# Kernel tuning notes

Hardware: AMD Instinct MI355X
Metric: run time of the kernel (lower is better)

## Reference

```python
import jax, jax.numpy as jnp
import numpy as np

B, L, D = 1, 512, 1280


def setup_inputs() -> dict:
    key = jax.random.key(0)
    k1, k2, k3 = jax.random.split(key, 3)
    prev_result = jax.random.normal(k1, (B, L, D), dtype=jnp.float32)
    # nn.Linear(2*D, 2): store weight as [2D, 2] so forward is x @ W + b
    W = jax.random.normal(k2, (2 * D, 2), dtype=jnp.float32) * (1.0 / np.sqrt(2 * D))
    b = jax.random.normal(k3, (2,), dtype=jnp.float32) * 0.01
    return {"prev_result": prev_result, "W": W, "b": b}


def reference(prev_result, W, b):
    # Dropout is identity at inference. The torch code builds
    # pairwise = cat(x_i * x_j, x_i - x_j) of shape [B,L,L,2D] then applies
    # Linear(2D, 2). We fuse: split W into the prod half Wp and diff half Wd.
    Wp, Wd = W[:D], W[D:]                                   # each [D, 2]
    # (x_i * x_j) @ Wp  -- bilinear contraction, no [B,L,L,2D] intermediate
    prod_term = jnp.einsum('bid,bjd,dk->bijk', prev_result, prev_result, Wp)
    # (x_i - x_j) @ Wd = (x @ Wd)_i - (x @ Wd)_j
    d_proj = prev_result @ Wd                                # [B, L, 2]
    diff_term = d_proj[:, :, None, :] - d_proj[:, None, :, :]
    prediction = prod_term + diff_term + b                   # [B, L, L, 2]
    prediction = (prediction + prediction.transpose(0, 2, 1, 3)) / 2
    return prediction[:, 1:-1, 1:-1]                         # [B, L-2, L-2, 2]
```

## Files before the change

kernel.cpp:

```cpp
#include <hip/hip_runtime.h>
#include <math.h>

#define D_DIM 1280
#define ODIM  510
#define KSTEPS 40

typedef short bf16x8 __attribute__((ext_vector_type(8)));
typedef float f32x4  __attribute__((ext_vector_type(4)));

__device__ __forceinline__ unsigned pkbf(float a, float b) {
  unsigned ua = __float_as_uint(a), ub = __float_as_uint(b);
  return ((ua + 0x8000u) >> 16) | ((ub + 0x8000u) & 0xffff0000u);
}

__global__ __launch_bounds__(256, 1) void pcmd_prep(
    const float* __restrict__ X,
    const float* __restrict__ W,
    unsigned short* __restrict__ Xbf,
    unsigned short* __restrict__ A0,
    unsigned short* __restrict__ A1)
{
  int T = (int)blockIdx.x * 256 + (int)threadIdx.x;
  int r = T / 160;
  int c = T - r * 160;
  const int K = c >> 2, quad = c & 3, m = r & 15, R = r >> 4;
  const size_t g = ((size_t)(R * KSTEPS + K) * 64 + quad * 16 + m) * 8;

  uint4 vx = {0,0,0,0}, v0 = {0,0,0,0}, v1 = {0,0,0,0};
  if (r <= 510) {
    const float* px = X + (size_t)(r + 1) * D_DIM + c * 8;
    float4 x0 = *(const float4*)px;
    float4 x1 = *(const float4*)(px + 4);
    const float* pw = W + (size_t)c * 16;
    float4 w0 = *(const float4*)(pw +  0);
    float4 w1 = *(const float4*)(pw +  4);
    float4 w2 = *(const float4*)(pw +  8);
    float4 w3 = *(const float4*)(pw + 12);
    vx.x = pkbf(x0.x, x0.y);            vx.y = pkbf(x0.z, x0.w);
    vx.z = pkbf(x1.x, x1.y);            vx.w = pkbf(x1.z, x1.w);
    v0.x = pkbf(x0.x*w0.x, x0.y*w0.z);  v0.y = pkbf(x0.z*w1.x, x0.w*w1.z);
    v0.z = pkbf(x1.x*w2.x, x1.y*w2.z);  v0.w = pkbf(x1.z*w3.x, x1.w*w3.z);
    v1.x = pkbf(x0.x*w0.y, x0.y*w0.w);  v1.y = pkbf(x0.z*w1.y, x0.w*w1.w);
    v1.z = pkbf(x1.x*w2.y, x1.y*w2.w);  v1.w = pkbf(x1.z*w3.y, x1.w*w3.w);
  }
  *(uint4*)(Xbf + g) = vx;
  *(uint4*)(A0  + g) = v0;
  *(uint4*)(A1  + g) = v1;
}

__global__ __launch_bounds__(256, 2) void pcmd_gemm(
    const unsigned short* __restrict__ Xbf,
    const unsigned short* __restrict__ A0,
    const unsigned short* __restrict__ A1,
    const float* __restrict__ b,
    float* __restrict__ out)
{
  __shared__ float sR[4][2][16][17];

  const int t = (int)blockIdx.x;
  int bi = (int)((65.0 - sqrt(4225.0 - 8.0 * (double)t)) * 0.5);
  {
    int s0 = bi * 32 - (bi * (bi - 1)) / 2;
    if (t < s0) { --bi; }
    int s1 = (bi + 1) * 32 - ((bi + 1) * bi) / 2;
    if (t >= s1) { ++bi; }
  }
  const int start = bi * 32 - (bi * (bi - 1)) / 2;
  const int bj = bi + (t - start);

  const int tid  = threadIdx.x;
  const int lane = tid & 63;
  const int wv   = tid >> 6;

  const unsigned short* pa0 = A0  + ((size_t)(bi * KSTEPS + wv * 10) * 64 + lane) * 8;
  const unsigned short* pa1 = A1  + ((size_t)(bi * KSTEPS + wv * 10) * 64 + lane) * 8;
  const unsigned short* pb  = Xbf + ((size_t)(bj * KSTEPS + wv * 10) * 64 + lane) * 8;

  bf16x8 ra0[4], ra1[4], rb[4];
  #pragma unroll
  for (int s = 0; s < 4; ++s) {
    ra0[s] = *(const bf16x8*)(pa0 + s * 512);
    ra1[s] = *(const bf16x8*)(pa1 + s * 512);
    rb[s]  = *(const bf16x8*)(pb  + s * 512);
  }

  f32x4 acc0 = {0.f, 0.f, 0.f, 0.f};
  f32x4 acc1 = {0.f, 0.f, 0.f, 0.f};

  #pragma unroll
  for (int s = 0; s < 10; ++s) {
    const int cur = s & 3;
    bf16x8 a0 = ra0[cur], a1 = ra1[cur], bb = rb[cur];
    if (s + 4 < 10) {
      ra0[cur] = *(const bf16x8*)(pa0 + (s + 4) * 512);
      ra1[cur] = *(const bf16x8*)(pa1 + (s + 4) * 512);
      rb[cur]  = *(const bf16x8*)(pb  + (s + 4) * 512);
    }
    acc0 = __builtin_amdgcn_mfma_f32_16x16x32_bf16(a0, bb, acc0, 0, 0, 0);
    acc1 = __builtin_amdgcn_mfma_f32_16x16x32_bf16(a1, bb, acc1, 0, 0, 0);
  }

  const int m = lane & 15, quad = lane >> 4;
  #pragma unroll
  for (int r = 0; r < 4; ++r) {
    sR[wv][0][quad * 4 + r][m] = acc0[r];
    sR[wv][1][quad * 4 + r][m] = acc1[r];
  }
  __syncthreads();

  const float b0 = b[0], b1 = b[1];
  const int il = tid >> 4, jl = tid & 15;

  {
    const int oi = bi * 16 + il, oj = bj * 16 + jl;
    if (oi < ODIM && oj < ODIM) {
      float2 v;
      v.x = sR[0][0][il][jl] + sR[1][0][il][jl] + sR[2][0][il][jl] + sR[3][0][il][jl] + b0;
      v.y = sR[0][1][il][jl] + sR[1][1][il][jl] + sR[2][1][il][jl] + sR[3][1][il][jl] + b1;
      *(float2*)(out + ((size_t)oi * ODIM + oj) * 2) = v;
    }
  }
  if (bi != bj) {
    const int oi = bj * 16 + il, oj = bi * 16 + jl;
    if (oi < ODIM && oj < ODIM) {
      float2 v;
      v.x = sR[0][0][jl][il] + sR[1][0][jl][il] + sR[2][0][jl][il] + sR[3][0][jl][il] + b0;
      v.y = sR[0][1][jl][il] + sR[1][1][jl][il] + sR[2][1][jl][il] + sR[3][1][jl][il] + b1;
      *(float2*)(out + ((size_t)oi * ODIM + oj) * 2) = v;
    }
  }
}

extern "C" void kernel_launch(void* const* d_in, const int* in_sizes, int n_in,
                              void* d_out, int out_size, void* d_ws, size_t ws_size,
                              hipStream_t stream) {
  const float* X = (const float*)d_in[0];
  const float* W = (const float*)d_in[1];
  const float* b = (const float*)d_in[2];
  float* out = (float*)d_out;
  (void)in_sizes; (void)n_in; (void)out_size; (void)ws_size;

  const size_t PLANE = (size_t)512 * D_DIM;
  unsigned short* Xbf = (unsigned short*)d_ws;
  unsigned short* A0  = Xbf + PLANE;
  unsigned short* A1  = A0 + PLANE;

  hipLaunchKernelGGL(pcmd_prep, dim3(320), dim3(256), 0, stream, X, W, Xbf, A0, A1);
  hipLaunchKernelGGL(pcmd_gemm, dim3(528), dim3(256), 0, stream, Xbf, A0, A1, b, out);
}
```

Baseline: 70.50 us.

## Fuse bf16 prep into GEMM kernel, converting X tiles on the fly via LDS

Drops the separate prep kernel that wrote bf16 X and weight-scaled A0/A1 planes to workspace. Each GEMM block now loads fp32 X rows for its i and j tiles directly, scales by W staged in shared memory, packs to bf16 into a swizzled LDS buffer, and feeds the MFMAs from there. This removes one kernel launch and the workspace round trip. In exchange each block re-reads and re-converts fp32 X (twice the bytes of bf16), and the global loads are no longer pipelined ahead of the MFMAs.

```diff
diff --git a/kernel.cpp b/kernel.cpp
--- a/kernel.cpp
+++ b/kernel.cpp
@@ -3,58 +3,24 @@
 
 #define D_DIM 1280
 #define ODIM  510
-#define KSTEPS 40
 
 typedef short bf16x8 __attribute__((ext_vector_type(8)));
 typedef float f32x4  __attribute__((ext_vector_type(4)));
+typedef unsigned uint2n __attribute__((ext_vector_type(2)));
 
 __device__ __forceinline__ unsigned pkbf(float a, float b) {
   unsigned ua = __float_as_uint(a), ub = __float_as_uint(b);
   return ((ua + 0x8000u) >> 16) | ((ub + 0x8000u) & 0xffff0000u);
 }
 
-__global__ __launch_bounds__(256, 1) void pcmd_prep(
+__global__ __launch_bounds__(256, 2) void pcmd_fused(
     const float* __restrict__ X,
     const float* __restrict__ W,
-    unsigned short* __restrict__ Xbf,
-    unsigned short* __restrict__ A0,
-    unsigned short* __restrict__ A1)
-{
-  int T = (int)blockIdx.x * 256 + (int)threadIdx.x;
-  int r = T / 160;
-  int c = T - r * 160;
-  const int K = c >> 2, quad = c & 3, m = r & 15, R = r >> 4;
-  const size_t g = ((size_t)(R * KSTEPS + K) * 64 + quad * 16 + m) * 8;
-
-  uint4 vx = {0,0,0,0}, v0 = {0,0,0,0}, v1 = {0,0,0,0};
-  if (r <= 510) {
-    const float* px = X + (size_t)(r + 1) * D_DIM + c * 8;
-    float4 x0 = *(const float4*)px;
-    float4 x1 = *(const float4*)(px + 4);
-    const float* pw = W + (size_t)c * 16;
-    float4 w0 = *(const float4*)(pw +  0);
-    float4 w1 = *(const float4*)(pw +  4);
-    float4 w2 = *(const float4*)(pw +  8);
-    float4 w3 = *(const float4*)(pw + 12);
-    vx.x = pkbf(x0.x, x0.y);            vx.y = pkbf(x0.z, x0.w);
-    vx.z = pkbf(x1.x, x1.y);            vx.w = pkbf(x1.z, x1.w);
-    v0.x = pkbf(x0.x*w0.x, x0.y*w0.z);  v0.y = pkbf(x0.z*w1.x, x0.w*w1.z);
-    v0.z = pkbf(x1.x*w2.x, x1.y*w2.z);  v0.w = pkbf(x1.z*w3.x, x1.w*w3.z);
-    v1.x = pkbf(x0.x*w0.y, x0.y*w0.w);  v1.y = pkbf(x0.z*w1.y, x0.w*w1.w);
-    v1.z = pkbf(x1.x*w2.y, x1.y*w2.w);  v1.w = pkbf(x1.z*w3.y, x1.w*w3.w);
-  }
-  *(uint4*)(Xbf + g) = vx;
-  *(uint4*)(A0  + g) = v0;
-  *(uint4*)(A1  + g) = v1;
-}
-
-__global__ __launch_bounds__(256, 2) void pcmd_gemm(
-    const unsigned short* __restrict__ Xbf,
-    const unsigned short* __restrict__ A0,
-    const unsigned short* __restrict__ A1,
     const float* __restrict__ b,
     float* __restrict__ out)
 {
+  __shared__ float sW[2 * D_DIM];
+  __shared__ unsigned short sF[4][3][5][64][8];
   __shared__ float sR[4][2][16][17];
 
   const int t = (int)blockIdx.x;
@@ -71,33 +37,76 @@
   const int tid  = threadIdx.x;
   const int lane = tid & 63;
   const int wv   = tid >> 6;
+  const int iT = bi * 16, jT = bj * 16;
 
-  const unsigned short* pa0 = A0  + ((size_t)(bi * KSTEPS + wv * 10) * 64 + lane) * 8;
-  const unsigned short* pa1 = A1  + ((size_t)(bi * KSTEPS + wv * 10) * 64 + lane) * 8;
-  const unsigned short* pb  = Xbf + ((size_t)(bj * KSTEPS + wv * 10) * 64 + lane) * 8;
-
-  bf16x8 ra0[4], ra1[4], rb[4];
-  #pragma unroll
-  for (int s = 0; s < 4; ++s) {
-    ra0[s] = *(const bf16x8*)(pa0 + s * 512);
-    ra1[s] = *(const bf16x8*)(pa1 + s * 512);
-    rb[s]  = *(const bf16x8*)(pb  + s * 512);
-  }
+  for (int i = tid; i < 640; i += 256)
+    *(float4*)(sW + i * 4) = *(const float4*)(W + i * 4);
+  __syncthreads();
 
   f32x4 acc0 = {0.f, 0.f, 0.f, 0.f};
   f32x4 acc1 = {0.f, 0.f, 0.f, 0.f};
 
-  #pragma unroll
-  for (int s = 0; s < 10; ++s) {
-    const int cur = s & 3;
-    bf16x8 a0 = ra0[cur], a1 = ra1[cur], bb = rb[cur];
-    if (s + 4 < 10) {
-      ra0[cur] = *(const bf16x8*)(pa0 + (s + 4) * 512);
-      ra1[cur] = *(const bf16x8*)(pa1 + (s + 4) * 512);
-      rb[cur]  = *(const bf16x8*)(pb  + (s + 4) * 512);
+  #pragma unroll 1
+  for (int ch = 0; ch < 2; ++ch) {
+    const int kb = wv * 320 + ch * 160;
+
+    float4 xb[10];
+    #pragma unroll
+    for (int tk = 0; tk < 10; ++tk) {
+      const int g = tk * 64 + lane;
+      const int lr = g / 40, c4 = g - lr * 40;
+      const int prow = jT + lr;
+      if (prow <= 509) xb[tk] = *(const float4*)(X + (size_t)(prow + 1) * D_DIM + kb + c4 * 4);
+      else             xb[tk] = make_float4(0.f, 0.f, 0.f, 0.f);
     }
-    acc0 = __builtin_amdgcn_mfma_f32_16x16x32_bf16(a0, bb, acc0, 0, 0, 0);
-    acc1 = __builtin_amdgcn_mfma_f32_16x16x32_bf16(a1, bb, acc1, 0, 0, 0);
+    #pragma unroll
+    for (int tk = 0; tk < 10; ++tk) {
+      const int g = tk * 64 + lane;
+      const int lr = g / 40, c4 = g - lr * 40;
+      const int s = c4 >> 3, quad = (c4 >> 1) & 3, half = c4 & 1;
+      const int rot = (lr + 5 * s) & 15;
+      uint2n u;
+      u.x = pkbf(xb[tk].x, xb[tk].y);
+      u.y = pkbf(xb[tk].z, xb[tk].w);
+      *(uint2n*)&sF[wv][0][s][quad * 16 + rot][half * 4] = u;
+    }
+
+    float4 xa[10], wqa[10], wqb[10];
+    #pragma unroll
+    for (int tk = 0; tk < 10; ++tk) {
+      const int g = tk * 64 + lane;
+      const int lr = g / 40, c4 = g - lr * 40;
+      const int prow = iT + lr;
+      if (prow <= 509) xa[tk] = *(const float4*)(X + (size_t)(prow + 1) * D_DIM + kb + c4 * 4);
+      else             xa[tk] = make_float4(0.f, 0.f, 0.f, 0.f);
+      const float* wp = sW + 2 * (kb + c4 * 4);
+      wqa[tk] = *(const float4*)wp;
+      wqb[tk] = *(const float4*)(wp + 4);
+    }
+    #pragma unroll
+    for (int tk = 0; tk < 10; ++tk) {
+      const int g = tk * 64 + lane;
+      const int lr = g / 40, c4 = g - lr * 40;
+      const int s = c4 >> 3, quad = (c4 >> 1) & 3, half = c4 & 1;
+      const int rot = (lr + 5 * s) & 15;
+      uint2n u0, u1;
+      u0.x = pkbf(xa[tk].x * wqa[tk].x, xa[tk].y * wqa[tk].z);
+      u0.y = pkbf(xa[tk].z * wqb[tk].x, xa[tk].w * wqb[tk].z);
+      u1.x = pkbf(xa[tk].x * wqa[tk].y, xa[tk].y * wqa[tk].w);
+      u1.y = pkbf(xa[tk].z * wqb[tk].y, xa[tk].w * wqb[tk].w);
+      *(uint2n*)&sF[wv][1][s][quad * 16 + rot][half * 4] = u0;
+      *(uint2n*)&sF[wv][2][s][quad * 16 + rot][half * 4] = u1;
+    }
+
+    #pragma unroll
+    for (int s = 0; s < 5; ++s) {
+      const int gq = (lane & 48) + (((lane & 15) + 5 * s) & 15);
+      bf16x8 fb  = *(const bf16x8*)&sF[wv][0][s][gq][0];
+      bf16x8 fa0 = *(const bf16x8*)&sF[wv][1][s][gq][0];
+      bf16x8 fa1 = *(const bf16x8*)&sF[wv][2][s][gq][0];
+      acc0 = __builtin_amdgcn_mfma_f32_16x16x32_bf16(fa0, fb, acc0, 0, 0, 0);
+      acc1 = __builtin_amdgcn_mfma_f32_16x16x32_bf16(fa1, fb, acc1, 0, 0, 0);
+    }
   }
 
   const int m = lane & 15, quad = lane >> 4;
@@ -112,7 +121,7 @@
   const int il = tid >> 4, jl = tid & 15;
 
   {
-    const int oi = bi * 16 + il, oj = bj * 16 + jl;
+    const int oi = iT + il, oj = jT + jl;
     if (oi < ODIM && oj < ODIM) {
       float2 v;
       v.x = sR[0][0][il][jl] + sR[1][0][il][jl] + sR[2][0][il][jl] + sR[3][0][il][jl] + b0;
@@ -121,7 +130,7 @@
     }
   }
   if (bi != bj) {
-    const int oi = bj * 16 + il, oj = bi * 16 + jl;
+    const int oi = jT + il, oj = iT + jl;
     if (oi < ODIM && oj < ODIM) {
       float2 v;
       v.x = sR[0][0][jl][il] + sR[1][0][jl][il] + sR[2][0][jl][il] + sR[3][0][jl][il] + b0;
@@ -138,13 +147,7 @@
   const float* W = (const float*)d_in[1];
   const float* b = (const float*)d_in[2];
   float* out = (float*)d_out;
-  (void)in_sizes; (void)n_in; (void)out_size; (void)ws_size;
+  (void)in_sizes; (void)n_in; (void)out_size; (void)d_ws; (void)ws_size;
 
-  const size_t PLANE = (size_t)512 * D_DIM;
-  unsigned short* Xbf = (unsigned short*)d_ws;
-  unsigned short* A0  = Xbf + PLANE;
-  unsigned short* A1  = A0 + PLANE;
-
-  hipLaunchKernelGGL(pcmd_prep, dim3(320), dim3(256), 0, stream, X, W, Xbf, A0, A1);
-  hipLaunchKernelGGL(pcmd_gemm, dim3(528), dim3(256), 0, stream, Xbf, A0, A1, b, out);
+  hipLaunchKernelGGL(pcmd_fused, dim3(528), dim3(256), 0, stream, X, W, b, out);
 }
```

After: 80.43 us. 14.1% more time.
